# Optimization experiments

Measured on AMD Instinct MI355X. Metric: run time of the kernel, lower is better.

The kernel has to match this reference:

```python
import jax, jax.numpy as jnp
import numpy as np

N_NODES = 50000
N_EDGES = 1_600_000
DIMS = [512, 256, 128]


def _edge_softmax(vals, rows, n):
    # sparse softmax over dim=1 (per source row), only over stored edges
    m = jax.ops.segment_max(vals, rows, num_segments=n)
    e = jnp.exp(vals - m[rows])
    s = jax.ops.segment_sum(e, rows, num_segments=n)
    return e / s[rows]


def _spmm(att, rows, cols, H, n):
    # (sparse C) @ H : gather source cols, scale by edge weight, scatter-add to rows
    return jax.ops.segment_sum(att[:, None] * H[cols], rows, num_segments=n)


def setup_inputs() -> dict:
    key = jax.random.key(0)
    ks = jax.random.split(key, 12)
    X = jax.random.normal(ks[0], (N_NODES, DIMS[0]), dtype=jnp.float32)
    edge_row = jax.random.randint(ks[1], (N_EDGES,), 0, N_NODES, dtype=jnp.int32)
    edge_col = jax.random.randint(ks[2], (N_EDGES,), 0, N_NODES, dtype=jnp.int32)
    A_vals = jnp.ones((N_EDGES,), dtype=jnp.float32)
    def lin(k, dout, din):
        lim = 1.0 / np.sqrt(din)
        return jax.random.uniform(k, (dout, din), jnp.float32, -lim, lim)
    W0 = lin(ks[3], DIMS[1], DIMS[0])
    b0 = jax.random.uniform(ks[4], (DIMS[1],), jnp.float32, -1/np.sqrt(DIMS[0]), 1/np.sqrt(DIMS[0]))
    W1 = lin(ks[5], DIMS[2], DIMS[1])
    b1 = jax.random.uniform(ks[6], (DIMS[2],), jnp.float32, -1/np.sqrt(DIMS[1]), 1/np.sqrt(DIMS[1]))
    v00 = jax.random.normal(ks[7], (DIMS[1],), dtype=jnp.float32)
    v01 = jax.random.normal(ks[8], (DIMS[1],), dtype=jnp.float32)
    v10 = jax.random.normal(ks[9], (DIMS[2],), dtype=jnp.float32)
    v11 = jax.random.normal(ks[10], (DIMS[2],), dtype=jnp.float32)
    return {"X": X, "edge_row": edge_row, "edge_col": edge_col, "A_vals": A_vals,
            "W0": W0, "b0": b0, "W1": W1, "b1": b1,
            "v00": v00, "v01": v01, "v10": v10, "v11": v11}


def reference(X, edge_row, edge_col, A_vals, W0, b0, W1, b1, v00, v01, v10, v11):
    n = X.shape[0]
    layers = [((W0, b0), (v00, v01)), ((W1, b1), (v10, v11))]
    H = X
    atts = []
    # encoder
    for (W, b), (va, vb) in layers:
        M = H @ W.T + b                               # [N, d_out]
        # attention logits are computed under no_grad in the original
        f1 = M @ va                                   # [N]
        f2 = M @ vb
        logits = jax.lax.stop_gradient(A_vals * (f1[edge_row] + f2[edge_col]))
        att = _edge_softmax(jax.nn.sigmoid(logits), edge_row, n)
        H = _spmm(att, edge_row, edge_col, M, n)
        atts.append(att)
    final_H = H
    # decoder (tied weights, reverse order, reuse encoder attention)
    for ((W, _), _), att in zip(reversed(layers), reversed(atts)):
        H = H @ W                                     # F.linear(H, W.t()) == H @ W
        H = _spmm(att, edge_row, edge_col, H, n)
    return H, final_H
```

## Files before the change

kernel.cpp:

```cpp
#include <hip/hip_runtime.h>
#include <cstdint>
#include <cstddef>

typedef __attribute__((ext_vector_type(8))) short bf16x8;
typedef __attribute__((ext_vector_type(4))) float f32x4;

__device__ __forceinline__ ushort f2b(float f) {
    union { float f; uint32_t u; } v; v.f = f;
    uint32_t r = (v.u + 0x7fffu + ((v.u >> 16) & 1u)) >> 16;
    return (ushort)r;
}
__device__ __forceinline__ float b2f(ushort b) {
    union { uint32_t u; float f; } v; v.u = ((uint32_t)b) << 16;
    return v.f;
}
__device__ __forceinline__ uint32_t pack2(float a, float b) {
    return (uint32_t)f2b(a) | ((uint32_t)f2b(b) << 16);
}
__device__ __forceinline__ float dot4(float4 a, float4 b) {
    return a.x * b.x + a.y * b.y + a.z * b.z + a.w * b.w;
}

__device__ __forceinline__ void gll16(const void* g, void* l) {
    __builtin_amdgcn_global_load_lds((const __attribute__((address_space(1))) void*)g,
                                     (__attribute__((address_space(3))) void*)l, 16, 0, 0);
}

__global__ __launch_bounds__(256) void hist_kernel(const int* __restrict__ rows,
                                                   int* __restrict__ bhist, int E, int nb) {
    __shared__ int h[512];
    for (int i = threadIdx.x; i < nb; i += 256) h[i] = 0;
    __syncthreads();
    int stride = gridDim.x * blockDim.x;
    for (int e = blockIdx.x * blockDim.x + threadIdx.x; e < E; e += stride)
        atomicAdd(&h[rows[e] >> 7], 1);
    __syncthreads();
    for (int i = threadIdx.x; i < nb; i += 256)
        if (h[i]) atomicAdd(&bhist[i], h[i]);
}

__global__ __launch_bounds__(512) void scan512(const int* __restrict__ bhist,
                                               int* __restrict__ boff, int* __restrict__ gcur,
                                               int* __restrict__ rp, int nb, int E, int N) {
    __shared__ int sm[512];
    int v = ((int)threadIdx.x < nb) ? bhist[threadIdx.x] : 0;
    sm[threadIdx.x] = v;
    __syncthreads();
    for (int off = 1; off < 512; off <<= 1) {
        int t = ((int)threadIdx.x >= off) ? sm[threadIdx.x - off] : 0;
        __syncthreads();
        sm[threadIdx.x] += t;
        __syncthreads();
    }
    if ((int)threadIdx.x < nb) {
        int e0 = sm[threadIdx.x] - v;
        boff[threadIdx.x] = e0;
        gcur[threadIdx.x] = e0;
    }
    if (threadIdx.x == 0) { boff[nb] = E; rp[N] = E; }
}

__global__ __launch_bounds__(256) void binpass(const int* __restrict__ rows,
                                               const int* __restrict__ cols,
                                               const float* __restrict__ avals,
                                               int* __restrict__ gcur,
                                               uint2* __restrict__ tmp, int E, int nb) {
    __shared__ int hist[512];
    __shared__ int base[512];
    int e0 = blockIdx.x * 4096;
    int nE = min(4096, E - e0);
    for (int i = threadIdx.x; i < nb; i += 256) hist[i] = 0;
    __syncthreads();
    for (int i = threadIdx.x; i < nE; i += 256)
        atomicAdd(&hist[rows[e0 + i] >> 7], 1);
    __syncthreads();
    for (int i = threadIdx.x; i < nb; i += 256) {
        int c = hist[i];
        if (c) base[i] = atomicAdd(&gcur[i], c);
        hist[i] = 0;
    }
    __syncthreads();
    for (int i = threadIdx.x; i < nE; i += 256) {
        int r = rows[e0 + i];
        int b = r >> 7;
        int loc = atomicAdd(&hist[b], 1);
        uint2 t;
        t.x = ((uint32_t)r << 16) | (uint32_t)cols[e0 + i];
        t.y = __float_as_uint(avals[e0 + i]);
        tmp[base[b] + loc] = t;
    }
}

__global__ __launch_bounds__(256) void bucketpass(const uint2* __restrict__ tmp,
                                                  const int* __restrict__ boff,
                                                  int* __restrict__ rp,
                                                  int* __restrict__ col_s,
                                                  float* __restrict__ a_s, int N) {
    __shared__ int cnt[128];
    __shared__ int pre[128];
    int b = blockIdx.x;
    int r0 = b << 7;
    int nr = min(128, N - r0);
    int t0 = boff[b], t1 = boff[b + 1];
    if ((int)threadIdx.x < 128) cnt[threadIdx.x] = 0;
    __syncthreads();
    for (int i = t0 + (int)threadIdx.x; i < t1; i += 256)
        atomicAdd(&cnt[(tmp[i].x >> 16) - r0], 1);
    __syncthreads();
    if ((int)threadIdx.x < 128) pre[threadIdx.x] = cnt[threadIdx.x];
    __syncthreads();
    for (int off = 1; off < 128; off <<= 1) {
        int t = ((int)threadIdx.x >= off && (int)threadIdx.x < 128) ? pre[threadIdx.x - off] : 0;
        __syncthreads();
        if ((int)threadIdx.x < 128) pre[threadIdx.x] += t;
        __syncthreads();
    }
    if ((int)threadIdx.x < nr) {
        int ex = pre[threadIdx.x] - cnt[threadIdx.x];
        rp[r0 + threadIdx.x] = t0 + ex;
        cnt[threadIdx.x] = t0 + ex;
    }
    __syncthreads();
    for (int i = t0 + (int)threadIdx.x; i < t1; i += 256) {
        uint2 t = tmp[i];
        int lr = (int)(t.x >> 16) - r0;
        int pos = atomicAdd(&cnt[lr], 1);
        col_s[pos] = (int)(t.x & 0xffffu);
        a_s[pos] = __uint_as_float(t.y);
    }
}

__global__ __launch_bounds__(256) void prep_all(const float* __restrict__ W0,
                                                const float* __restrict__ W1,
                                                const float* __restrict__ b0,
                                                const float* __restrict__ v00,
                                                const float* __restrict__ v01,
                                                ushort* __restrict__ W1h,
                                                ushort* __restrict__ Wt0h,
                                                float* __restrict__ u0,
                                                float* __restrict__ u1,
                                                float* __restrict__ bp,
                                                float* __restrict__ cc) {
    __shared__ float su0[256];
    __shared__ float su1[256];
    int bid = blockIdx.x;
    int tid = threadIdx.x;
    if (bid < 128) {
        int i = bid * 256 + tid;
        float4 v = ((const float4*)W0)[i];
        ushort4 o;
        o.x = f2b(v.x); o.y = f2b(v.y); o.z = f2b(v.z); o.w = f2b(v.w);
        int r = (i * 4) >> 9;
        int c = (i * 4) & 511;
        Wt0h[(size_t)(c + 0) * 256 + r] = o.x;
        Wt0h[(size_t)(c + 1) * 256 + r] = o.y;
        Wt0h[(size_t)(c + 2) * 256 + r] = o.z;
        Wt0h[(size_t)(c + 3) * 256 + r] = o.w;
        if (i < 8192) {
            float4 w = ((const float4*)W1)[i];
            ushort4 p;
            p.x = f2b(w.x); p.y = f2b(w.y); p.z = f2b(w.z); p.w = f2b(w.w);
            ((ushort4*)W1h)[i] = p;
        }
    } else if (bid < 144) {
        int ci = tid & 31;
        int rl = tid >> 5;
        int c = (bid - 128) * 32 + ci;
        float s0 = 0.f, s1 = 0.f;
        for (int r = rl; r < 256; r += 8) {
            float w = W0[(size_t)r * 512 + c];
            s0 += w * v00[r];
            s1 += w * v01[r];
        }
        su0[tid] = s0;
        su1[tid] = s1;
        __syncthreads();
        if (tid < 32) {
            float a = 0.f, b = 0.f;
            for (int g = 0; g < 8; ++g) { a += su0[g * 32 + tid]; b += su1[g * 32 + tid]; }
            u0[c] = a;
            u1[c] = b;
        }
    } else {
        int i = tid;
        if (i < 128) {
            float s = 0.f;
            for (int k = 0; k < 256; ++k) s += W1[(size_t)i * 256 + k] * b0[k];
            bp[i] = s;
        } else if (i == 128) {
            float s = 0.f;
            for (int k = 0; k < 256; ++k) s += b0[k] * v00[k];
            cc[0] = s;
        } else if (i == 129) {
            float s = 0.f;
            for (int k = 0; k < 256; ++k) s += b0[k] * v01[k];
            cc[1] = s;
        }
    }
}

__global__ __launch_bounds__(256) void gemm_bf16(const ushort* __restrict__ A,
                                                 const ushort* __restrict__ B,
                                                 const float* __restrict__ bias,
                                                 float* __restrict__ Cf,
                                                 ushort* __restrict__ Ch,
                                                 ushort* __restrict__ ChT,
                                                 int M, int K, int Dout) {
    __shared__ ushort As[128 * 64];
    __shared__ ushort Bs[128 * 64];
    int bm = blockIdx.y * 128, bn = blockIdx.x * 128;
    int tid = threadIdx.x;
    int w = tid >> 6, l = tid & 63;
    int wm = (w & 1) * 64, wn = (w >> 1) * 64;
    int lm = l & 15, quad = l >> 4;
    int wslot = tid & 192;

    f32x4 acc[4][4] = {};

    for (int k0 = 0; k0 < K; k0 += 64) {
#pragma unroll
        for (int it = 0; it < 4; ++it) {
            int slot = it * 256 + tid;
            int row = slot >> 3;
            int qg = ((slot & 7) ^ (row & 7)) * 8;
            int ga = bm + row; if (ga > M - 1) ga = M - 1;
            gll16(A + (size_t)ga * K + k0 + qg, As + (size_t)(it * 256 + wslot) * 8);
            gll16(B + (size_t)(bn + row) * K + k0 + qg, Bs + (size_t)(it * 256 + wslot) * 8);
        }
        __syncthreads();
#pragma unroll
        for (int ks = 0; ks < 2; ++ks) {
            bf16x8 af[4], bfr[4];
#pragma unroll
            for (int i = 0; i < 4; ++i) {
                int r = wm + i * 16 + lm;
                af[i] = *(const bf16x8*)&As[r * 64 + (((ks * 4 + quad) ^ (r & 7)) * 8)];
            }
#pragma unroll
            for (int j = 0; j < 4; ++j) {
                int r = wn + j * 16 + lm;
                bfr[j] = *(const bf16x8*)&Bs[r * 64 + (((ks * 4 + quad) ^ (r & 7)) * 8)];
            }
#pragma unroll
            for (int i = 0; i < 4; ++i)
#pragma unroll
                for (int j = 0; j < 4; ++j)
                    acc[i][j] = __builtin_amdgcn_mfma_f32_16x16x32_bf16(af[i], bfr[j], acc[i][j], 0, 0, 0);
        }
        __syncthreads();
    }

    float bv[4] = {0.f, 0.f, 0.f, 0.f};
    if (bias) {
#pragma unroll
        for (int j = 0; j < 4; ++j) bv[j] = bias[bn + wn + j * 16 + lm];
    }
#pragma unroll
    for (int i = 0; i < 4; ++i) {
#pragma unroll
        for (int r = 0; r < 4; ++r) {
            int row = bm + wm + i * 16 + quad * 4 + r;
            if (row < M) {
#pragma unroll
                for (int j = 0; j < 4; ++j) {
                    int col = bn + wn + j * 16 + lm;
                    float v = acc[i][j][r] + bv[j];
                    if (Cf) Cf[(size_t)row * Dout + col] = v;
                    if (Ch) Ch[(size_t)row * Dout + col] = f2b(v);
                    if (ChT) ChT[(size_t)col * M + row] = f2b(v);
                }
            }
        }
    }
}

__global__ __launch_bounds__(256) void gemm_xp(const float* __restrict__ X,
                                               const ushort* __restrict__ B,
                                               const float* __restrict__ bp,
                                               const float* __restrict__ u0,
                                               const float* __restrict__ u1,
                                               const float* __restrict__ cc,
                                               ushort* __restrict__ Ph,
                                               float* __restrict__ f1,
                                               float* __restrict__ f2,
                                               int M, int K) {
    __shared__ ushort As[128 * 64];
    __shared__ ushort Bs[128 * 64];
    int bm = blockIdx.y * 128;
    int tid = threadIdx.x;
    int w = tid >> 6, l = tid & 63;
    int wm = (w & 1) * 64, wn = (w >> 1) * 64;
    int lm = l & 15, quad = l >> 4;
    int wslot = tid & 192;
    int ar = tid >> 2;
    int aq = tid & 3;

    f32x4 acc[4][4] = {};
    float fA1 = 0.f, fA2 = 0.f, fB1 = 0.f, fB2 = 0.f;

    for (int k0 = 0; k0 < K; k0 += 64) {
#pragma unroll
        for (int it = 0; it < 4; ++it) {
            int slot = it * 256 + tid;
            int row = slot >> 3;
            int qg = ((slot & 7) ^ (row & 7)) * 8;
            gll16(B + (size_t)row * K + k0 + qg, Bs + (size_t)(it * 256 + wslot) * 8);
        }
        const float4* U0 = (const float4*)(u0 + k0 + aq * 16);
        const float4* U1 = (const float4*)(u1 + k0 + aq * 16);
        float4 ua0 = U0[0], ua1 = U0[1], ua2 = U0[2], ua3 = U0[3];
        float4 va0 = U1[0], va1 = U1[1], va2 = U1[2], va3 = U1[3];
#pragma unroll
        for (int rr = 0; rr < 2; ++rr) {
            int row = ar + rr * 64;
            int ga = bm + row; if (ga > M - 1) ga = M - 1;
            const float4* src = (const float4*)(X + (size_t)ga * K + k0 + aq * 16);
            float4 x0 = src[0], x1 = src[1], x2 = src[2], x3 = src[3];
            float s1 = dot4(x0, ua0) + dot4(x1, ua1) + dot4(x2, ua2) + dot4(x3, ua3);
            float s2 = dot4(x0, va0) + dot4(x1, va1) + dot4(x2, va2) + dot4(x3, va3);
            if (rr == 0) { fA1 += s1; fA2 += s2; } else { fB1 += s1; fB2 += s2; }
            uint4 pa, pb;
            pa.x = pack2(x0.x, x0.y); pa.y = pack2(x0.z, x0.w);
            pa.z = pack2(x1.x, x1.y); pa.w = pack2(x1.z, x1.w);
            pb.x = pack2(x2.x, x2.y); pb.y = pack2(x2.z, x2.w);
            pb.z = pack2(x3.x, x3.y); pb.w = pack2(x3.z, x3.w);
            int c0 = (aq * 2) ^ (row & 7);
            int c1 = (aq * 2 + 1) ^ (row & 7);
            *(uint4*)&As[row * 64 + c0 * 8] = pa;
            *(uint4*)&As[row * 64 + c1 * 8] = pb;
        }
        __syncthreads();
#pragma unroll
        for (int ks = 0; ks < 2; ++ks) {
            bf16x8 af[4], bfr[4];
#pragma unroll
            for (int i = 0; i < 4; ++i) {
                int r = wm + i * 16 + lm;
                af[i] = *(const bf16x8*)&As[r * 64 + (((ks * 4 + quad) ^ (r & 7)) * 8)];
            }
#pragma unroll
            for (int j = 0; j < 4; ++j) {
                int r = wn + j * 16 + lm;
                bfr[j] = *(const bf16x8*)&Bs[r * 64 + (((ks * 4 + quad) ^ (r & 7)) * 8)];
            }
#pragma unroll
            for (int i = 0; i < 4; ++i)
#pragma unroll
                for (int j = 0; j < 4; ++j)
                    acc[i][j] = __builtin_amdgcn_mfma_f32_16x16x32_bf16(af[i], bfr[j], acc[i][j], 0, 0, 0);
        }
        __syncthreads();
    }

    fA1 += __shfl_xor(fA1, 1); fA1 += __shfl_xor(fA1, 2);
    fA2 += __shfl_xor(fA2, 1); fA2 += __shfl_xor(fA2, 2);
    fB1 += __shfl_xor(fB1, 1); fB1 += __shfl_xor(fB1, 2);
    fB2 += __shfl_xor(fB2, 1); fB2 += __shfl_xor(fB2, 2);
    if (aq == 0) {
        float c0 = cc[0], c1 = cc[1];
        int r0 = bm + ar;
        if (r0 < M) { f1[r0] = fA1 + c0; f2[r0] = fA2 + c1; }
        int r1 = r0 + 64;
        if (r1 < M) { f1[r1] = fB1 + c0; f2[r1] = fB2 + c1; }
    }

    float bv[4];
#pragma unroll
    for (int j = 0; j < 4; ++j) bv[j] = bp[wn + j * 16 + lm];
#pragma unroll
    for (int i = 0; i < 4; ++i) {
#pragma unroll
        for (int r = 0; r < 4; ++r) {
            int row = bm + wm + i * 16 + quad * 4 + r;
            if (row < M) {
#pragma unroll
                for (int j = 0; j < 4; ++j) {
                    int col = wn + j * 16 + lm;
                    Ph[(size_t)row * 128 + col] = f2b(acc[i][j][r] + bv[j]);
                }
            }
        }
    }
}

__global__ __launch_bounds__(256) void att2_kernel(const int* __restrict__ rp,
                                                   const int* __restrict__ col_s,
                                                   const float* __restrict__ a_s,
                                                   const float* __restrict__ f1,
                                                   const float* __restrict__ f2,
                                                   float* __restrict__ att,
                                                   float* __restrict__ rs, int N) {
    int r = blockIdx.x * 4 + (threadIdx.x >> 6);
    if (r >= N) return;
    int lane = threadIdx.x & 63;
    int beg = rp[r], end = rp[r + 1];
    float fr = f1[r];
    float s = 0.f;
    for (int j = beg + lane; j < end; j += 64) {
        float x = a_s[j] * (fr + f2[col_s[j]]);
        float v = 1.f / (1.f + __expf(-x));
        float e = __expf(v);
        att[j] = e;
        s += e;
    }
#pragma unroll
    for (int off = 32; off > 0; off >>= 1) s += __shfl_xor(s, off);
    if (lane == 0) rs[r] = (end > beg) ? 1.f / s : 0.f;
}

__global__ __launch_bounds__(256) void spmm128(const int* __restrict__ rp,
                                               const int* __restrict__ col_s,
                                               const float* __restrict__ att,
                                               const float* __restrict__ rs,
                                               const ushort* __restrict__ H,
                                               const float* __restrict__ bias,
                                               const float* __restrict__ va,
                                               const float* __restrict__ vb,
                                               float* __restrict__ f1,
                                               float* __restrict__ f2,
                                               ushort* __restrict__ Oh,
                                               float* __restrict__ Of, int N) {
    int r = blockIdx.x * 16 + (threadIdx.x >> 4);
    if (r >= N) return;
    int lane = threadIdx.x & 15;
    int beg = rp[r], end = rp[r + 1];
    float acc[8] = {0.f, 0.f, 0.f, 0.f, 0.f, 0.f, 0.f, 0.f};
    const uint4* H4 = (const uint4*)H;
#define FMA8(h, wgt) { \
        acc[0] += (wgt) * b2f((ushort)((h).x & 0xffffu)); \
        acc[1] += (wgt) * b2f((ushort)((h).x >> 16)); \
        acc[2] += (wgt) * b2f((ushort)((h).y & 0xffffu)); \
        acc[3] += (wgt) * b2f((ushort)((h).y >> 16)); \
        acc[4] += (wgt) * b2f((ushort)((h).z & 0xffffu)); \
        acc[5] += (wgt) * b2f((ushort)((h).z >> 16)); \
        acc[6] += (wgt) * b2f((ushort)((h).w & 0xffffu)); \
        acc[7] += (wgt) * b2f((ushort)((h).w >> 16)); }
    int j = beg;
    for (; j + 8 <= end; j += 8) {
        int c0 = col_s[j],     c1 = col_s[j + 1], c2 = col_s[j + 2], c3 = col_s[j + 3];
        int c4 = col_s[j + 4], c5 = col_s[j + 5], c6 = col_s[j + 6], c7 = col_s[j + 7];
        float w0 = att[j],     w1 = att[j + 1], w2 = att[j + 2], w3 = att[j + 3];
        float w4 = att[j + 4], w5 = att[j + 5], w6 = att[j + 6], w7 = att[j + 7];
        uint4 h0 = H4[(size_t)c0 * 16 + lane];
        uint4 h1 = H4[(size_t)c1 * 16 + lane];
        uint4 h2 = H4[(size_t)c2 * 16 + lane];
        uint4 h3 = H4[(size_t)c3 * 16 + lane];
        uint4 h4 = H4[(size_t)c4 * 16 + lane];
        uint4 h5 = H4[(size_t)c5 * 16 + lane];
        uint4 h6 = H4[(size_t)c6 * 16 + lane];
        uint4 h7 = H4[(size_t)c7 * 16 + lane];
        FMA8(h0, w0) FMA8(h1, w1) FMA8(h2, w2) FMA8(h3, w3)
        FMA8(h4, w4) FMA8(h5, w5) FMA8(h6, w6) FMA8(h7, w7)
    }
    for (; j + 4 <= end; j += 4) {
        int c0 = col_s[j], c1 = col_s[j + 1], c2 = col_s[j + 2], c3 = col_s[j + 3];
        float w0 = att[j], w1 = att[j + 1], w2 = att[j + 2], w3 = att[j + 3];
        uint4 h0 = H4[(size_t)c0 * 16 + lane];
        uint4 h1 = H4[(size_t)c1 * 16 + lane];
        uint4 h2 = H4[(size_t)c2 * 16 + lane];
        uint4 h3 = H4[(size_t)c3 * 16 + lane];
        FMA8(h0, w0) FMA8(h1, w1) FMA8(h2, w2) FMA8(h3, w3)
    }
    for (; j < end; ++j) {
        uint4 h = H4[(size_t)col_s[j] * 16 + lane];
        float w0 = att[j];
        FMA8(h, w0)
    }
#undef FMA8
    float rsv = rs[r];
#pragma unroll
    for (int k = 0; k < 8; ++k) acc[k] *= rsv;
    if (bias) {
        const float4* b4 = (const float4*)(bias + lane * 8);
        float4 ba = b4[0], bb = b4[1];
        acc[0] += ba.x; acc[1] += ba.y; acc[2] += ba.z; acc[3] += ba.w;
        acc[4] += bb.x; acc[5] += bb.y; acc[6] += bb.z; acc[7] += bb.w;
    }
    if (va) {
        const float4* a4 = (const float4*)(va + lane * 8);
        const float4* c4 = (const float4*)(vb + lane * 8);
        float4 va0 = a4[0], va1 = a4[1], vb0 = c4[0], vb1 = c4[1];
        float p1 = acc[0] * va0.x + acc[1] * va0.y + acc[2] * va0.z + acc[3] * va0.w
                 + acc[4] * va1.x + acc[5] * va1.y + acc[6] * va1.z + acc[7] * va1.w;
        float p2 = acc[0] * vb0.x + acc[1] * vb0.y + acc[2] * vb0.z + acc[3] * vb0.w
                 + acc[4] * vb1.x + acc[5] * vb1.y + acc[6] * vb1.z + acc[7] * vb1.w;
#pragma unroll
        for (int off = 8; off > 0; off >>= 1) {
            p1 += __shfl_xor(p1, off);
            p2 += __shfl_xor(p2, off);
        }
        if (lane == 0) { f1[r] = p1; f2[r] = p2; }
    }
    if (Oh) {
        uint4 o;
        o.x = (uint32_t)f2b(acc[0]) | ((uint32_t)f2b(acc[1]) << 16);
        o.y = (uint32_t)f2b(acc[2]) | ((uint32_t)f2b(acc[3]) << 16);
        o.z = (uint32_t)f2b(acc[4]) | ((uint32_t)f2b(acc[5]) << 16);
        o.w = (uint32_t)f2b(acc[6]) | ((uint32_t)f2b(acc[7]) << 16);
        ((uint4*)Oh)[(size_t)r * 16 + lane] = o;
    }
    if (Of) {
        float4* O4 = (float4*)Of;
        O4[(size_t)r * 32 + lane * 2]     = make_float4(acc[0], acc[1], acc[2], acc[3]);
        O4[(size_t)r * 32 + lane * 2 + 1] = make_float4(acc[4], acc[5], acc[6], acc[7]);
    }
}

extern "C" void kernel_launch(void* const* d_in, const int* in_sizes, int n_in,
                              void* d_out, int out_size, void* d_ws, size_t ws_size,
                              hipStream_t stream) {
    const float* X    = (const float*)d_in[0];
    const int*   erow = (const int*)d_in[1];
    const int*   ecol = (const int*)d_in[2];
    const float* aval = (const float*)d_in[3];
    const float* W0   = (const float*)d_in[4];
    const float* b0   = (const float*)d_in[5];
    const float* W1   = (const float*)d_in[6];
    const float* b1   = (const float*)d_in[7];
    const float* v00  = (const float*)d_in[8];
    const float* v01  = (const float*)d_in[9];
    const float* v10  = (const float*)d_in[10];
    const float* v11  = (const float*)d_in[11];

    const int D0 = 512, D1 = 256, D2 = 128;
    const int N = in_sizes[0] / D0;
    const int E = in_sizes[1];
    const int NB = (N + 127) / 128;
    float* out = (float*)d_out;

    char* ws = (char*)d_ws;
    size_t off = 0;
    auto alloc = [&](size_t bytes) {
        char* p = ws + off;
        off += (bytes + 255) & ~(size_t)255;
        return p;
    };
    ushort* Ph   = (ushort*)alloc((size_t)N * D2 * 2);
    ushort* M1h  = (ushort*)alloc((size_t)N * D2 * 2);
    ushort* H2h  = (ushort*)alloc((size_t)N * D2 * 2);
    ushort* S0h  = (ushort*)alloc((size_t)N * D2 * 2);
    ushort* W1h  = (ushort*)alloc((size_t)D2 * D1 * 2);
    ushort* Wt0h = (ushort*)alloc((size_t)D0 * D1 * 2);
    ushort* Wph  = (ushort*)alloc((size_t)D2 * D0 * 2);
    ushort* WfTh = (ushort*)alloc((size_t)D0 * D2 * 2);
    float* att0  = (float*)alloc((size_t)E * 4);
    float* att1  = (float*)alloc((size_t)E * 4);
    float* a_s   = (float*)alloc((size_t)E * 4);
    float* f1    = (float*)alloc((size_t)N * 4);
    float* f2    = (float*)alloc((size_t)N * 4);
    float* rs0   = (float*)alloc((size_t)N * 4);
    float* rs1   = (float*)alloc((size_t)N * 4);
    float* u0    = (float*)alloc(512 * 4);
    float* u1    = (float*)alloc(512 * 4);
    float* bp    = (float*)alloc(128 * 4);
    float* cc    = (float*)alloc(2 * 4);
    int* rp      = (int*)alloc(((size_t)N + 1) * 4);
    int* col_s   = (int*)alloc((size_t)E * 4);
    uint2* tmp   = (uint2*)alloc((size_t)E * 8);
    int* bhist   = (int*)alloc(512 * 4);
    int* boff    = (int*)alloc(513 * 4);
    int* gcur    = (int*)alloc(512 * 4);

    hipMemsetAsync(bhist, 0, 512 * sizeof(int), stream);
    hist_kernel<<<256, 256, 0, stream>>>(erow, bhist, E, NB);
    scan512<<<1, 512, 0, stream>>>(bhist, boff, gcur, rp, NB, E, N);
    binpass<<<(E + 4095) / 4096, 256, 0, stream>>>(erow, ecol, aval, gcur, tmp, E, NB);
    bucketpass<<<NB, 256, 0, stream>>>(tmp, boff, rp, col_s, a_s, N);

    prep_all<<<145, 256, 0, stream>>>(W0, W1, b0, v00, v01, W1h, Wt0h, u0, u1, bp, cc);

    gemm_bf16<<<dim3(4, 1), 256, 0, stream>>>(W1h, Wt0h, nullptr, nullptr, Wph, WfTh,
                                              D2, D1, D0);

    const int gy = (N + 127) / 128;
    const int agrid = (N + 3) / 4;
    const int sgrid = (N + 15) / 16;

    gemm_xp<<<dim3(1, gy), 256, 0, stream>>>(X, Wph, bp, u0, u1, cc, Ph, f1, f2, N, D0);
    att2_kernel<<<agrid, 256, 0, stream>>>(rp, col_s, a_s, f1, f2, att0, rs0, N);
    spmm128<<<sgrid, 256, 0, stream>>>(rp, col_s, att0, rs0, Ph, b1, v10, v11, f1, f2,
                                       M1h, nullptr, N);
    att2_kernel<<<agrid, 256, 0, stream>>>(rp, col_s, a_s, f1, f2, att1, rs1, N);
    spmm128<<<sgrid, 256, 0, stream>>>(rp, col_s, att1, rs1, M1h, nullptr,
                                       nullptr, nullptr, nullptr, nullptr,
                                       H2h, out + (size_t)N * D0, N);

    spmm128<<<sgrid, 256, 0, stream>>>(rp, col_s, att1, rs1, H2h, nullptr,
                                       nullptr, nullptr, nullptr, nullptr,
                                       Ph, nullptr, N);
    spmm128<<<sgrid, 256, 0, stream>>>(rp, col_s, att0, rs0, Ph, nullptr,
                                       nullptr, nullptr, nullptr, nullptr,
                                       S0h, nullptr, N);
    gemm_bf16<<<dim3(D0 / 128, gy), 256, 0, stream>>>(S0h, WfTh, nullptr, out, nullptr,
                                                      nullptr, N, D2, D0);
}
```

Baseline: 612.6 us.

## Fuse edge attention computation into encoder SpMM kernels

```diff
diff --git a/kernel.cpp b/kernel.cpp
--- a/kernel.cpp
+++ b/kernel.cpp
@@ -383,49 +383,6 @@
     }
 }
 
-__global__ __launch_bounds__(256) void att2_kernel(const int* __restrict__ rp,
-                                                   const int* __restrict__ col_s,
-                                                   const float* __restrict__ a_s,
-                                                   const float* __restrict__ f1,
-                                                   const float* __restrict__ f2,
-                                                   float* __restrict__ att,
-                                                   float* __restrict__ rs, int N) {
-    int r = blockIdx.x * 4 + (threadIdx.x >> 6);
-    if (r >= N) return;
-    int lane = threadIdx.x & 63;
-    int beg = rp[r], end = rp[r + 1];
-    float fr = f1[r];
-    float s = 0.f;
-    for (int j = beg + lane; j < end; j += 64) {
-        float x = a_s[j] * (fr + f2[col_s[j]]);
-        float v = 1.f / (1.f + __expf(-x));
-        float e = __expf(v);
-        att[j] = e;
-        s += e;
-    }
-#pragma unroll
-    for (int off = 32; off > 0; off >>= 1) s += __shfl_xor(s, off);
-    if (lane == 0) rs[r] = (end > beg) ? 1.f / s : 0.f;
-}
-
-__global__ __launch_bounds__(256) void spmm128(const int* __restrict__ rp,
-                                               const int* __restrict__ col_s,
-                                               const float* __restrict__ att,
-                                               const float* __restrict__ rs,
-                                               const ushort* __restrict__ H,
-                                               const float* __restrict__ bias,
-                                               const float* __restrict__ va,
-                                               const float* __restrict__ vb,
-                                               float* __restrict__ f1,
-                                               float* __restrict__ f2,
-                                               ushort* __restrict__ Oh,
-                                               float* __restrict__ Of, int N) {
-    int r = blockIdx.x * 16 + (threadIdx.x >> 4);
-    if (r >= N) return;
-    int lane = threadIdx.x & 15;
-    int beg = rp[r], end = rp[r + 1];
-    float acc[8] = {0.f, 0.f, 0.f, 0.f, 0.f, 0.f, 0.f, 0.f};
-    const uint4* H4 = (const uint4*)H;
 #define FMA8(h, wgt) { \
         acc[0] += (wgt) * b2f((ushort)((h).x & 0xffffu)); \
         acc[1] += (wgt) * b2f((ushort)((h).x >> 16)); \
@@ -435,6 +392,127 @@
         acc[5] += (wgt) * b2f((ushort)((h).z >> 16)); \
         acc[6] += (wgt) * b2f((ushort)((h).w & 0xffffu)); \
         acc[7] += (wgt) * b2f((ushort)((h).w >> 16)); }
+
+__global__ __launch_bounds__(256) void spmm_att(const int* __restrict__ rp,
+                                                const int* __restrict__ col_s,
+                                                const float* __restrict__ a_s,
+                                                const float* __restrict__ fin1,
+                                                const float* __restrict__ fin2,
+                                                float* __restrict__ attOut,
+                                                float* __restrict__ rsOut,
+                                                const ushort* __restrict__ H,
+                                                const float* __restrict__ bias,
+                                                const float* __restrict__ va,
+                                                const float* __restrict__ vb,
+                                                float* __restrict__ g1,
+                                                float* __restrict__ g2,
+                                                ushort* __restrict__ Oh,
+                                                float* __restrict__ Of, int N) {
+    int r = blockIdx.x * 16 + (threadIdx.x >> 4);
+    if (r >= N) return;
+    int lane = threadIdx.x & 15;
+    int kl = lane & 7;
+    int gb = threadIdx.x & 48;
+    int beg = rp[r], end = rp[r + 1];
+    float fr = fin1[r];
+    float ssum = 0.f;
+    float acc[8] = {0.f, 0.f, 0.f, 0.f, 0.f, 0.f, 0.f, 0.f};
+    const uint4* H4 = (const uint4*)H;
+    int j = beg;
+    for (; j + 8 <= end; j += 8) {
+        int   cL = col_s[j + kl];
+        float aL = a_s[j + kl];
+        float xL = aL * (fr + fin2[cL]);
+        float eL = __expf(1.f / (1.f + __expf(-xL)));
+        if (lane < 8) { attOut[j + lane] = eL; ssum += eL; }
+        float w0 = __shfl(eL, gb + 0), w1 = __shfl(eL, gb + 1);
+        float w2 = __shfl(eL, gb + 2), w3 = __shfl(eL, gb + 3);
+        float w4 = __shfl(eL, gb + 4), w5 = __shfl(eL, gb + 5);
+        float w6 = __shfl(eL, gb + 6), w7 = __shfl(eL, gb + 7);
+        int c0 = col_s[j],     c1 = col_s[j + 1], c2 = col_s[j + 2], c3 = col_s[j + 3];
+        int c4 = col_s[j + 4], c5 = col_s[j + 5], c6 = col_s[j + 6], c7 = col_s[j + 7];
+        uint4 h0 = H4[(size_t)c0 * 16 + lane];
+        uint4 h1 = H4[(size_t)c1 * 16 + lane];
+        uint4 h2 = H4[(size_t)c2 * 16 + lane];
+        uint4 h3 = H4[(size_t)c3 * 16 + lane];
+        uint4 h4 = H4[(size_t)c4 * 16 + lane];
+        uint4 h5 = H4[(size_t)c5 * 16 + lane];
+        uint4 h6 = H4[(size_t)c6 * 16 + lane];
+        uint4 h7 = H4[(size_t)c7 * 16 + lane];
+        FMA8(h0, w0) FMA8(h1, w1) FMA8(h2, w2) FMA8(h3, w3)
+        FMA8(h4, w4) FMA8(h5, w5) FMA8(h6, w6) FMA8(h7, w7)
+    }
+    int rem = end - j;
+    if (rem > 0) {
+        bool valid = kl < rem;
+        int   cL = col_s[valid ? j + kl : beg];
+        float aL = valid ? a_s[j + kl] : 0.f;
+        float xL = aL * (fr + fin2[cL]);
+        float eL = valid ? __expf(1.f / (1.f + __expf(-xL))) : 0.f;
+        if (lane < 8 && valid) { attOut[j + lane] = eL; ssum += eL; }
+        for (int k = 0; k < rem; ++k) {
+            float wk = __shfl(eL, gb + k);
+            int ck = col_s[j + k];
+            uint4 hk = H4[(size_t)ck * 16 + lane];
+            FMA8(hk, wk)
+        }
+    }
+    ssum += __shfl_xor(ssum, 1);
+    ssum += __shfl_xor(ssum, 2);
+    ssum += __shfl_xor(ssum, 4);
+    ssum += __shfl_xor(ssum, 8);
+    float rsv = (end > beg) ? 1.f / ssum : 0.f;
+    if (lane == 0) rsOut[r] = rsv;
+#pragma unroll
+    for (int k = 0; k < 8; ++k) acc[k] *= rsv;
+    if (bias) {
+        const float4* b4 = (const float4*)(bias + lane * 8);
+        float4 ba = b4[0], bb = b4[1];
+        acc[0] += ba.x; acc[1] += ba.y; acc[2] += ba.z; acc[3] += ba.w;
+        acc[4] += bb.x; acc[5] += bb.y; acc[6] += bb.z; acc[7] += bb.w;
+    }
+    if (va) {
+        const float4* a4 = (const float4*)(va + lane * 8);
+        const float4* c4 = (const float4*)(vb + lane * 8);
+        float4 va0 = a4[0], va1 = a4[1], vb0 = c4[0], vb1 = c4[1];
+        float p1 = acc[0] * va0.x + acc[1] * va0.y + acc[2] * va0.z + acc[3] * va0.w
+                 + acc[4] * va1.x + acc[5] * va1.y + acc[6] * va1.z + acc[7] * va1.w;
+        float p2 = acc[0] * vb0.x + acc[1] * vb0.y + acc[2] * vb0.z + acc[3] * vb0.w
+                 + acc[4] * vb1.x + acc[5] * vb1.y + acc[6] * vb1.z + acc[7] * vb1.w;
+#pragma unroll
+        for (int off = 8; off > 0; off >>= 1) {
+            p1 += __shfl_xor(p1, off);
+            p2 += __shfl_xor(p2, off);
+        }
+        if (lane == 0) { g1[r] = p1; g2[r] = p2; }
+    }
+    if (Oh) {
+        uint4 o;
+        o.x = (uint32_t)f2b(acc[0]) | ((uint32_t)f2b(acc[1]) << 16);
+        o.y = (uint32_t)f2b(acc[2]) | ((uint32_t)f2b(acc[3]) << 16);
+        o.z = (uint32_t)f2b(acc[4]) | ((uint32_t)f2b(acc[5]) << 16);
+        o.w = (uint32_t)f2b(acc[6]) | ((uint32_t)f2b(acc[7]) << 16);
+        ((uint4*)Oh)[(size_t)r * 16 + lane] = o;
+    }
+    if (Of) {
+        float4* O4 = (float4*)Of;
+        O4[(size_t)r * 32 + lane * 2]     = make_float4(acc[0], acc[1], acc[2], acc[3]);
+        O4[(size_t)r * 32 + lane * 2 + 1] = make_float4(acc[4], acc[5], acc[6], acc[7]);
+    }
+}
+
+__global__ __launch_bounds__(256) void spmm128(const int* __restrict__ rp,
+                                               const int* __restrict__ col_s,
+                                               const float* __restrict__ att,
+                                               const float* __restrict__ rs,
+                                               const ushort* __restrict__ H,
+                                               ushort* __restrict__ Oh, int N) {
+    int r = blockIdx.x * 16 + (threadIdx.x >> 4);
+    if (r >= N) return;
+    int lane = threadIdx.x & 15;
+    int beg = rp[r], end = rp[r + 1];
+    float acc[8] = {0.f, 0.f, 0.f, 0.f, 0.f, 0.f, 0.f, 0.f};
+    const uint4* H4 = (const uint4*)H;
     int j = beg;
     for (; j + 8 <= end; j += 8) {
         int c0 = col_s[j],     c1 = col_s[j + 1], c2 = col_s[j + 2], c3 = col_s[j + 3];
@@ -452,59 +530,22 @@
         FMA8(h0, w0) FMA8(h1, w1) FMA8(h2, w2) FMA8(h3, w3)
         FMA8(h4, w4) FMA8(h5, w5) FMA8(h6, w6) FMA8(h7, w7)
     }
-    for (; j + 4 <= end; j += 4) {
-        int c0 = col_s[j], c1 = col_s[j + 1], c2 = col_s[j + 2], c3 = col_s[j + 3];
-        float w0 = att[j], w1 = att[j + 1], w2 = att[j + 2], w3 = att[j + 3];
-        uint4 h0 = H4[(size_t)c0 * 16 + lane];
-        uint4 h1 = H4[(size_t)c1 * 16 + lane];
-        uint4 h2 = H4[(size_t)c2 * 16 + lane];
-        uint4 h3 = H4[(size_t)c3 * 16 + lane];
-        FMA8(h0, w0) FMA8(h1, w1) FMA8(h2, w2) FMA8(h3, w3)
-    }
     for (; j < end; ++j) {
         uint4 h = H4[(size_t)col_s[j] * 16 + lane];
         float w0 = att[j];
         FMA8(h, w0)
     }
+    float rsv = rs[r];
+#pragma unroll
+    for (int k = 0; k < 8; ++k) acc[k] *= rsv;
+    uint4 o;
+    o.x = (uint32_t)f2b(acc[0]) | ((uint32_t)f2b(acc[1]) << 16);
+    o.y = (uint32_t)f2b(acc[2]) | ((uint32_t)f2b(acc[3]) << 16);
+    o.z = (uint32_t)f2b(acc[4]) | ((uint32_t)f2b(acc[5]) << 16);
+    o.w = (uint32_t)f2b(acc[6]) | ((uint32_t)f2b(acc[7]) << 16);
+    ((uint4*)Oh)[(size_t)r * 16 + lane] = o;
+}
 #undef FMA8
-    float rsv = rs[r];
-#pragma unroll
-    for (int k = 0; k < 8; ++k) acc[k] *= rsv;
-    if (bias) {
-        const float4* b4 = (const float4*)(bias + lane * 8);
-        float4 ba = b4[0], bb = b4[1];
-        acc[0] += ba.x; acc[1] += ba.y; acc[2] += ba.z; acc[3] += ba.w;
-        acc[4] += bb.x; acc[5] += bb.y; acc[6] += bb.z; acc[7] += bb.w;
-    }
-    if (va) {
-        const float4* a4 = (const float4*)(va + lane * 8);
-        const float4* c4 = (const float4*)(vb + lane * 8);
-        float4 va0 = a4[0], va1 = a4[1], vb0 = c4[0], vb1 = c4[1];
-        float p1 = acc[0] * va0.x + acc[1] * va0.y + acc[2] * va0.z + acc[3] * va0.w
-                 + acc[4] * va1.x + acc[5] * va1.y + acc[6] * va1.z + acc[7] * va1.w;
-        float p2 = acc[0] * vb0.x + acc[1] * vb0.y + acc[2] * vb0.z + acc[3] * vb0.w
-                 + acc[4] * vb1.x + acc[5] * vb1.y + acc[6] * vb1.z + acc[7] * vb1.w;
-#pragma unroll
-        for (int off = 8; off > 0; off >>= 1) {
-            p1 += __shfl_xor(p1, off);
-            p2 += __shfl_xor(p2, off);
-        }
-        if (lane == 0) { f1[r] = p1; f2[r] = p2; }
-    }
-    if (Oh) {
-        uint4 o;
-        o.x = (uint32_t)f2b(acc[0]) | ((uint32_t)f2b(acc[1]) << 16);
-        o.y = (uint32_t)f2b(acc[2]) | ((uint32_t)f2b(acc[3]) << 16);
-        o.z = (uint32_t)f2b(acc[4]) | ((uint32_t)f2b(acc[5]) << 16);
-        o.w = (uint32_t)f2b(acc[6]) | ((uint32_t)f2b(acc[7]) << 16);
-        ((uint4*)Oh)[(size_t)r * 16 + lane] = o;
-    }
-    if (Of) {
-        float4* O4 = (float4*)Of;
-        O4[(size_t)r * 32 + lane * 2]     = make_float4(acc[0], acc[1], acc[2], acc[3]);
-        O4[(size_t)r * 32 + lane * 2 + 1] = make_float4(acc[4], acc[5], acc[6], acc[7]);
-    }
-}
 
 extern "C" void kernel_launch(void* const* d_in, const int* in_sizes, int n_in,
                               void* d_out, int out_size, void* d_ws, size_t ws_size,
@@ -548,6 +589,8 @@
     float* a_s   = (float*)alloc((size_t)E * 4);
     float* f1    = (float*)alloc((size_t)N * 4);
     float* f2    = (float*)alloc((size_t)N * 4);
+    float* g1    = (float*)alloc((size_t)N * 4);
+    float* g2    = (float*)alloc((size_t)N * 4);
     float* rs0   = (float*)alloc((size_t)N * 4);
     float* rs1   = (float*)alloc((size_t)N * 4);
     float* u0    = (float*)alloc(512 * 4);
@@ -573,24 +616,17 @@
                                               D2, D1, D0);
 
     const int gy = (N + 127) / 128;
-    const int agrid = (N + 3) / 4;
     const int sgrid = (N + 15) / 16;
 
     gemm_xp<<<dim3(1, gy), 256, 0, stream>>>(X, Wph, bp, u0, u1, cc, Ph, f1, f2, N, D0);
-    att2_kernel<<<agrid, 256, 0, stream>>>(rp, col_s, a_s, f1, f2, att0, rs0, N);
-    spmm128<<<sgrid, 256, 0, stream>>>(rp, col_s, att0, rs0, Ph, b1, v10, v11, f1, f2,
-                                       M1h, nullptr, N);
-    att2_kernel<<<agrid, 256, 0, stream>>>(rp, col_s, a_s, f1, f2, att1, rs1, N);
-    spmm128<<<sgrid, 256, 0, stream>>>(rp, col_s, att1, rs1, M1h, nullptr,
-                                       nullptr, nullptr, nullptr, nullptr,
-                                       H2h, out + (size_t)N * D0, N);
-
-    spmm128<<<sgrid, 256, 0, stream>>>(rp, col_s, att1, rs1, H2h, nullptr,
-                                       nullptr, nullptr, nullptr, nullptr,
-                                       Ph, nullptr, N);
-    spmm128<<<sgrid, 256, 0, stream>>>(rp, col_s, att0, rs0, Ph, nullptr,
-                                       nullptr, nullptr, nullptr, nullptr,
-                                       S0h, nullptr, N);
+    spmm_att<<<sgrid, 256, 0, stream>>>(rp, col_s, a_s, f1, f2, att0, rs0,
+                                        Ph, b1, v10, v11, g1, g2, M1h, nullptr, N);
+    spmm_att<<<sgrid, 256, 0, stream>>>(rp, col_s, a_s, g1, g2, att1, rs1,
+                                        M1h, nullptr, nullptr, nullptr, nullptr, nullptr,
+                                        H2h, out + (size_t)N * D0, N);
+
+    spmm128<<<sgrid, 256, 0, stream>>>(rp, col_s, att1, rs1, H2h, Ph, N);
+    spmm128<<<sgrid, 256, 0, stream>>>(rp, col_s, att0, rs0, Ph, S0h, N);
     gemm_bf16<<<dim3(D0 / 128, gy), 256, 0, stream>>>(S0h, WfTh, nullptr, out, nullptr,
                                                       nullptr, N, D2, D0);
 }
```

New measurement: 611.7 us. No clear change (-0.2%).
